# Optimization experiments

Hardware: AMD Instinct MI355X
Metric: run time of the kernel (lower is better)

The kernel has to match this reference:

```python
import jax, jax.numpy as jnp
from jax import lax
import numpy as np

BN_INV = 1.0 / np.sqrt(1.0 + 1e-5)  # eval-mode BatchNorm with running mean 0, var 1


def gather_points(x, idx):
    # x: [B, N, C]; idx: [B, ...] int -> [B, ..., C]
    bi = jnp.arange(x.shape[0]).reshape((x.shape[0],) + (1,) * (idx.ndim - 1))
    return x[bi, idx]


def fps(xyz, npoint):
    # furthest point sampling starting at index 0. xyz: [B, N, 3] -> [B, npoint] int32
    B, N, _ = xyz.shape

    def step(carry, _):
        dist, last = carry
        lx = jnp.take_along_axis(xyz, last[:, None, None], axis=1)  # [B,1,3]
        d = jnp.sum((xyz - lx) ** 2, axis=-1)                       # [B,N]
        dist = jnp.minimum(dist, d)
        nxt = jnp.argmax(dist, axis=-1).astype(jnp.int32)
        return (dist, nxt), nxt

    first = jnp.zeros((B,), jnp.int32)
    dist0 = jnp.full((B, N), 1e10, xyz.dtype)
    _, rest = lax.scan(step, (dist0, first), None, length=npoint - 1)
    return jnp.concatenate([first[None], rest], axis=0).T  # [B, npoint]


def ball_query(radius, nsample, xyz, new_xyz):
    # first nsample points (in index order) within radius of each query; pad with first hit
    N = xyz.shape[1]
    d2 = jnp.sum((new_xyz[:, :, None, :] - xyz[:, None, :, :]) ** 2, axis=-1)  # [B,S,N]
    mask = d2 < radius * radius
    key = jnp.where(mask, jnp.arange(N, dtype=jnp.int32), N)
    idx_sorted = jnp.sort(key, axis=-1)[..., :nsample]                          # [B,S,ns]
    cnt = jnp.sum(mask, axis=-1, keepdims=True)                                 # [B,S,1]
    idx = jnp.where(jnp.arange(nsample) < cnt, idx_sorted, idx_sorted[..., :1])
    return jnp.minimum(idx, N - 1)


def bn_relu(x, gamma, beta):
    # eval-mode BN (running mean 0 / var 1) + ReLU; channels on the last axis
    return jax.nn.relu(x * (gamma * BN_INV) + beta)


def sa_module(xyz, feats, npoint, radius, nsample, layers):
    # xyz [B,N,3], feats [B,C,N] -> (new_xyz [B,S,3], new_feats [B,Cout,S])
    fidx = fps(xyz, npoint)
    new_xyz = gather_points(xyz, fidx)                      # [B,S,3]
    gidx = ball_query(radius, nsample, xyz, new_xyz)        # [B,S,ns]
    g_xyz = gather_points(xyz, gidx) - new_xyz[:, :, None, :]   # [B,S,ns,3]
    g_feat = gather_points(jnp.swapaxes(feats, 1, 2), gidx)     # [B,S,ns,C]
    h = jnp.concatenate([g_xyz, g_feat], axis=-1)               # use_xyz=True
    for (w, g, b) in layers:                                    # shared MLP (1x1 conv2d+BN+ReLU)
        h = bn_relu(jnp.einsum('bsnc,oc->bsno', h, w), g, b)
    return new_xyz, jnp.swapaxes(jnp.max(h, axis=2), 1, 2)      # max-pool over nsample


def fp_module(unk_xyz, kn_xyz, unk_feats, kn_feats, layers):
    # three-NN weighted interpolation (squared distances, as the CUDA op) + unit conv MLP
    d2 = jnp.sum((unk_xyz[:, :, None, :] - kn_xyz[:, None, :, :]) ** 2, axis=-1)
    neg, idx = lax.top_k(-d2, 3)                 # 3 nearest known points
    w = 1.0 / (-neg + 1e-8)
    w = w / jnp.sum(w, axis=-1, keepdims=True)   # [B,Nu,3]
    kf = gather_points(jnp.swapaxes(kn_feats, 1, 2), idx)       # [B,Nu,3,C]
    interp = jnp.sum(kf * w[..., None], axis=2)                 # [B,Nu,C]
    h = jnp.concatenate([interp, jnp.swapaxes(unk_feats, 1, 2)], axis=-1)
    for (wt, g, b) in layers:
        h = bn_relu(jnp.einsum('bnc,oc->bno', h, wt), g, b)
    return jnp.swapaxes(h, 1, 2)                                # [B,Cout,Nu]


def setup_inputs() -> dict:
    key = jax.random.key(0)
    it = iter(jax.random.split(key, 80))
    B, N = 16, 4096
    d = {
        'xyz': jax.random.uniform(next(it), (B, N, 3), jnp.float32) * 0.3,
        'feats': jax.random.normal(next(it), (B, N, 3), jnp.float32),
    }
    specs = {'sa1': [(6, 64), (64, 128)], 'sa2': [(131, 128), (128, 256)],
             'sa3': [(259, 256), (256, 512)], 'fp3': [(768, 256), (256, 256)],
             'fp2': [(384, 128), (128, 128)], 'fp1': [(131, 128), (128, 128)]}
    for name, layers in specs.items():
        for i, (ci, co) in enumerate(layers):
            d[f'{name}_w{i}'] = jax.random.normal(next(it), (co, ci), jnp.float32) / np.sqrt(ci)
            d[f'{name}_g{i}'] = 1.0 + 0.1 * jax.random.normal(next(it), (co,), jnp.float32)
            d[f'{name}_b{i}'] = 0.1 * jax.random.normal(next(it), (co,), jnp.float32)
    d['fin_w'] = jax.random.normal(next(it), (512, 128), jnp.float32) / np.sqrt(128.0)
    d['fin_b'] = 0.1 * jax.random.normal(next(it), (512,), jnp.float32)
    d['fin_g'] = 1.0 + 0.1 * jax.random.normal(next(it), (512,), jnp.float32)
    d['fin_be'] = 0.1 * jax.random.normal(next(it), (512,), jnp.float32)
    return d


def reference(xyz, feats,
              sa1_w0, sa1_g0, sa1_b0, sa1_w1, sa1_g1, sa1_b1,
              sa2_w0, sa2_g0, sa2_b0, sa2_w1, sa2_g1, sa2_b1,
              sa3_w0, sa3_g0, sa3_b0, sa3_w1, sa3_g1, sa3_b1,
              fp3_w0, fp3_g0, fp3_b0, fp3_w1, fp3_g1, fp3_b1,
              fp2_w0, fp2_g0, fp2_b0, fp2_w1, fp2_g1, fp2_b1,
              fp1_w0, fp1_g0, fp1_b0, fp1_w1, fp1_g1, fp1_b1,
              fin_w, fin_b, fin_g, fin_be):
    f0 = jnp.swapaxes(feats, 1, 2)  # [B,3,N], channel-first like the torch module
    l1x, l1f = sa_module(xyz, f0, 256, 0.04, 16,
                         [(sa1_w0, sa1_g0, sa1_b0), (sa1_w1, sa1_g1, sa1_b1)])
    l2x, l2f = sa_module(l1x, l1f, 64, 0.08, 16,
                         [(sa2_w0, sa2_g0, sa2_b0), (sa2_w1, sa2_g1, sa2_b1)])
    l3x, l3f = sa_module(l2x, l2f, 16, 0.16, 16,
                         [(sa3_w0, sa3_g0, sa3_b0), (sa3_w1, sa3_g1, sa3_b1)])
    l2f = fp_module(l2x, l3x, l2f, l3f, [(fp3_w0, fp3_g0, fp3_b0), (fp3_w1, fp3_g1, fp3_b1)])
    l1f = fp_module(l1x, l2x, l1f, l2f, [(fp2_w0, fp2_g0, fp2_b0), (fp2_w1, fp2_g1, fp2_b1)])
    l0f = fp_module(xyz, l1x, f0, l1f, [(fp1_w0, fp1_g0, fp1_b0), (fp1_w1, fp1_g1, fp1_b1)])
    # final Conv1d(128->512, bias) + BN + ReLU
    h = jnp.einsum('bcn,oc->bon', l0f, fin_w) + fin_b[None, :, None]
    h = jax.nn.relu(h * (fin_g * BN_INV)[None, :, None] + fin_be[None, :, None])
    B, C, N = h.shape
    return jnp.swapaxes(h, 1, 2).reshape(B * N, C)  # un-batched per-point features
```

## Files before the change

### kernel.cpp

```cpp
#include <hip/hip_runtime.h>

#define DEVI __device__ __forceinline__
typedef unsigned long long u64;

static constexpr float BN_INV_F = 0.9999950000374997f;

DEVI float d2rn(float ax, float ay, float az, float bx, float by, float bz) {
    float dx = __fsub_rn(ax, bx), dy = __fsub_rn(ay, by), dz = __fsub_rn(az, bz);
    return __fadd_rn(__fadd_rn(__fmul_rn(dx, dx), __fmul_rn(dy, dy)), __fmul_rn(dz, dz));
}

DEVI u64 shfl_xor_u64(u64 x, int m) {
    unsigned lo = (unsigned)x, hi = (unsigned)(x >> 32);
    lo = (unsigned)__shfl_xor((int)lo, m, 64);
    hi = (unsigned)__shfl_xor((int)hi, m, 64);
    return ((u64)hi << 32) | lo;
}
DEVI u64 umin64(u64 a, u64 b) { return a < b ? a : b; }
DEVI u64 umax64(u64 a, u64 b) { return a > b ? a : b; }

template <int N, int NPOINT, int BS>
__global__ __launch_bounds__(BS) void fps_kernel(const float* __restrict__ xyz,
                                                 int* __restrict__ fidx) {
    constexpr int PPT = N / BS;
    constexpr int NW = BS / 64;
    __shared__ float xsx[N], xsy[N], xsz[N];
    __shared__ u64 wmax[2][NW > 0 ? NW : 1];
    const int t = threadIdx.x, b = blockIdx.x, lane = t & 63, wv = t >> 6;
    const float* xb = xyz + (size_t)b * N * 3;
    for (int p = t; p < N; p += BS) {
        xsx[p] = xb[p * 3]; xsy[p] = xb[p * 3 + 1]; xsz[p] = xb[p * 3 + 2];
    }
    float dist[PPT];
#pragma unroll
    for (int i = 0; i < PPT; ++i) dist[i] = 1e10f;
    if (t == 0) fidx[b * NPOINT] = 0;
    __syncthreads();
    float qx = xsx[0], qy = xsy[0], qz = xsz[0];
    for (int it = 1; it < NPOINT; ++it) {
        u64 best = 0ull;
#pragma unroll
        for (int i = 0; i < PPT; ++i) {
            int p = i * BS + t;
            float d = d2rn(xsx[p], xsy[p], xsz[p], qx, qy, qz);
            float nd = fminf(dist[i], d);
            dist[i] = nd;
            u64 pk = ((u64)__float_as_uint(nd) << 32) | (unsigned)(0xFFFFFFFFu - (unsigned)p);
            if (pk > best) best = pk;
        }
#pragma unroll
        for (int m = 1; m < 64; m <<= 1) best = umax64(best, shfl_xor_u64(best, m));
        if constexpr (NW > 1) {
            if (lane == 0) wmax[it & 1][wv] = best;
            __syncthreads();
            u64 m2 = wmax[it & 1][lane & (NW - 1)];
#pragma unroll
            for (int m = 1; m < NW; m <<= 1) m2 = umax64(m2, shfl_xor_u64(m2, m));
            best = m2;
        }
        int p = (int)(0xFFFFFFFFu - (unsigned)best);
        qx = xsx[p]; qy = xsy[p]; qz = xsz[p];
        if (t == 0) fidx[b * NPOINT + it] = p;
    }
}

template <int TR, int XSTR, int CI, int CO, int MODE>
DEVI void gemm_phase(float* __restrict__ Xs, float* __restrict__ Ws,
                     const float* __restrict__ W,
                     const float* __restrict__ sA, const float* __restrict__ sB,
                     const float* __restrict__ fbias,
                     float* __restrict__ gout, int r0,
                     unsigned* __restrict__ mp, int t) {
    constexpr int RT = TR / 16;
    constexpr int NCOL = (CO / 16 < 8) ? (CO / 16) : 8;
    constexpr int ROWS = 16 * NCOL;
    constexpr int CC = CO / ROWS;
    constexpr int CI16 = ((CI + 15) / 16) * 16;
    constexpr int NCH = CI16 / 8;
    constexpr int NQ = CC * NCH;
    constexpr int PRE = ROWS * 8 / 256;
    constexpr int XSTR4 = XSTR / 4;
    constexpr int AC = (MODE == 0) ? CC : 1;
    const int tx = t & 15, ty = t >> 4;
    float acc[AC][RT][NCOL];
    if constexpr (MODE == 0) {
#pragma unroll
        for (int a = 0; a < AC; ++a)
#pragma unroll
            for (int r = 0; r < RT; ++r)
#pragma unroll
                for (int i = 0; i < NCOL; ++i) acc[a][r][i] = 0.f;
    }
    float pre[PRE];
#pragma unroll
    for (int i = 0; i < PRE; ++i) {
        int e = t + 256 * i, row = e >> 3, kk = e & 7;
        pre[i] = (kk < CI) ? W[(size_t)row * CI + kk] : 0.f;
    }
#pragma unroll
    for (int i = 0; i < PRE; ++i) {
        int e = t + 256 * i;
        Ws[(e >> 3) * 12 + (e & 7)] = pre[i];
    }
#pragma unroll
    for (int cc = 0; cc < CC; ++cc) {
        if constexpr (MODE != 0) {
#pragma unroll
            for (int r = 0; r < RT; ++r)
#pragma unroll
                for (int i = 0; i < NCOL; ++i) acc[0][r][i] = 0.f;
        }
        for (int kc = 0; kc < NCH; ++kc) {
            const int qq = cc * NCH + kc, buf = kc & 1;
            __syncthreads();
            if (qq + 1 < NQ) {
                const int cn = (qq + 1) / NCH, kn = ((qq + 1) % NCH) * 8;
#pragma unroll
                for (int i = 0; i < PRE; ++i) {
                    int e = t + 256 * i, row = e >> 3, k = kn + (e & 7);
                    pre[i] = (k < CI) ? W[(size_t)(cn * ROWS + row) * CI + k] : 0.f;
                }
            }
            const float* wsb = Ws + buf * 1536;
#pragma unroll
            for (int k4i = 0; k4i < 2; ++k4i) {
                const int c4 = kc * 2 + k4i;
                float4 wv[NCOL];
#pragma unroll
                for (int i = 0; i < NCOL; ++i)
                    wv[i] = *(const float4*)&wsb[(tx + 16 * i) * 12 + k4i * 4];
#pragma unroll
                for (int r = 0; r < RT; ++r) {
                    float4 xv = *(const float4*)
                        &Xs[(((ty * RT + r) * XSTR4) + (c4 ^ (ty & 3))) * 4];
                    float* A;
                    if constexpr (MODE == 0) A = acc[cc][r]; else A = acc[0][r];
#pragma unroll
                    for (int i = 0; i < NCOL; ++i) {
                        A[i] = fmaf(xv.x, wv[i].x, A[i]);
                        A[i] = fmaf(xv.y, wv[i].y, A[i]);
                        A[i] = fmaf(xv.z, wv[i].z, A[i]);
                        A[i] = fmaf(xv.w, wv[i].w, A[i]);
                    }
                }
            }
            if (qq + 1 < NQ) {
                float* wsn = Ws + (buf ^ 1) * 1536;
#pragma unroll
                for (int i = 0; i < PRE; ++i) {
                    int e = t + 256 * i;
                    wsn[(e >> 3) * 12 + (e & 7)] = pre[i];
                }
            }
        }
        if constexpr (MODE == 1) {
#pragma unroll
            for (int i = 0; i < NCOL; ++i) {
                int c = cc * ROWS + tx + 16 * i;
                float bia = fbias[c], sc = sA[c] * BN_INV_F, be = sB[c];
#pragma unroll
                for (int r = 0; r < RT; ++r) {
                    float val = fmaxf(fmaf(acc[0][r][i] + bia, sc, be), 0.f);
                    gout[(size_t)(r0 + ty * RT + r) * CO + c] = val;
                }
            }
        } else if constexpr (MODE == 2) {
#pragma unroll
            for (int i = 0; i < NCOL; ++i) {
                int c = cc * ROWS + tx + 16 * i;
                float sc = sA[c] * BN_INV_F, bb = sB[c];
#pragma unroll
                for (int r = 0; r < RT; ++r) {
                    float val = fmaxf(fmaf(acc[0][r][i], sc, bb), 0.f);
                    atomicMax(&mp[((ty * RT + r) >> 4) * CO + c], __float_as_uint(val));
                }
            }
        }
    }
    if constexpr (MODE == 0) {
        __syncthreads();
#pragma unroll
        for (int cc = 0; cc < CC; ++cc)
#pragma unroll
            for (int i = 0; i < NCOL; ++i) {
                int c = cc * ROWS + tx + 16 * i;
                float sc = sA[c] * BN_INV_F, bb = sB[c];
#pragma unroll
                for (int r = 0; r < RT; ++r) {
                    int row = ty * RT + r;
                    Xs[(row * XSTR4 + ((c >> 2) ^ (ty & 3))) * 4 + (c & 3)] =
                        fmaxf(fmaf(acc[cc][r][i], sc, bb), 0.f);
                }
            }
        __syncthreads();
    }
}

template <int N, int S, int CIN, int C1, int C2, int TR>
__global__ __launch_bounds__(256) void sa_kernel(
    const float* __restrict__ xyz, const float* __restrict__ feats,
    const int* __restrict__ fidx,
    const float* __restrict__ w0, const float* __restrict__ g0, const float* __restrict__ b0,
    const float* __restrict__ w1, const float* __restrict__ g1, const float* __restrict__ b1,
    float* __restrict__ oxyz, float* __restrict__ ofeat, float r2) {
    constexpr int QPB = TR / 16;
    constexpr int C = 3 + CIN;
    constexpr int CI16 = ((C + 15) / 16) * 16;
    constexpr int XSTR = (CI16 > C1) ? CI16 : C1;
    constexpr int XSTR4 = XSTR / 4;
    constexpr int RTl = TR / 16;
    __shared__ __align__(16) float Xs[TR * XSTR];
    __shared__ __align__(16) float Ws[2 * 128 * 12];
    __shared__ int ids[QPB][16];
    __shared__ float qp[QPB][3];
    __shared__ unsigned mp[(TR / 16) * C2];
    const int t = threadIdx.x, lane = t & 63, wv = t >> 6;
    const int q0 = blockIdx.x * QPB;
    for (int q = wv; q < QPB; q += 4) {
        const int sq = q0 + q, bb = sq / S;
        const float* xb = xyz + (size_t)bb * N * 3;
        const int qi = fidx[sq];
        const float qx = xb[qi * 3], qy = xb[qi * 3 + 1], qz = xb[qi * 3 + 2];
        if (lane == 0) {
            qp[q][0] = qx; qp[q][1] = qy; qp[q][2] = qz;
            float* op = oxyz + (size_t)sq * 3;
            op[0] = qx; op[1] = qy; op[2] = qz;
        }
        int base = 0;
        for (int seg = 0; seg < N; seg += 64) {
            const int p = seg + lane;
            float d = d2rn(xb[p * 3], xb[p * 3 + 1], xb[p * 3 + 2], qx, qy, qz);
            bool hit = d < r2;
            u64 mask = __ballot(hit);
            int before = (int)__popcll(mask & ((1ull << lane) - 1ull));
            if (hit && base + before < 16) ids[q][base + before] = p;
            base += (int)__popcll(mask);
            if (base >= 16) break;
        }
        if (lane == 0) {
            int cnt = base < 16 ? base : 16;
            int first = ids[q][0];
            for (int r = cnt; r < 16; ++r) ids[q][r] = first;
        }
    }
    __syncthreads();
    if constexpr (CIN == 3) {
        for (int e = t; e < TR * CI16; e += 256) {
            int j = e / CI16, c = e % CI16;
            int q = j >> 4, p = ids[q][j & 15];
            int bb = (q0 + q) / S;
            float v = 0.f;
            if (c < 3) v = __fsub_rn(xyz[((size_t)bb * N + p) * 3 + c], qp[q][c]);
            else if (c < C) v = feats[((size_t)bb * N + p) * CIN + (c - 3)];
            Xs[(j * XSTR4 + ((c >> 2) ^ ((j / RTl) & 3))) * 4 + (c & 3)] = v;
        }
    } else {
        for (int e = t; e < TR * 16; e += 256) {
            int j = e / 16, ci = e % 16;
            int q = j >> 4, p = ids[q][j & 15];
            int bb = (q0 + q) / S;
            int c = (ci < 3) ? ci : (C + ci - 3);
            if (c >= CI16) continue;
            float v = (ci < 3) ? __fsub_rn(xyz[((size_t)bb * N + p) * 3 + ci], qp[q][ci]) : 0.f;
            Xs[(j * XSTR4 + ((c >> 2) ^ ((j / RTl) & 3))) * 4 + (c & 3)] = v;
        }
        for (int e = t; e < TR * (CIN / 4); e += 256) {
            int j = e / (CIN / 4), c4i = e % (CIN / 4);
            int q = j >> 4, p = ids[q][j & 15];
            int bb = (q0 + q) / S;
            float4 v = *(const float4*)&feats[((size_t)bb * N + p) * CIN + c4i * 4];
            int sw = (j / RTl) & 3;
            float vv[4] = {v.x, v.y, v.z, v.w};
#pragma unroll
            for (int u = 0; u < 4; ++u) {
                int c = 3 + c4i * 4 + u;
                Xs[(j * XSTR4 + ((c >> 2) ^ sw)) * 4 + (c & 3)] = vv[u];
            }
        }
    }
    gemm_phase<TR, XSTR, C, C1, 0>(Xs, Ws, w0, g0, b0, nullptr, nullptr, 0, nullptr, t);
    for (int e = t; e < (TR / 16) * C2; e += 256) mp[e] = 0u;
    gemm_phase<TR, XSTR, C1, C2, 2>(Xs, Ws, w1, g1, b1, nullptr, nullptr, 0, mp, t);
    __syncthreads();
    for (int e = t; e < QPB * C2; e += 256) {
        int q = e / C2, c = e % C2;
        ofeat[(size_t)(q0 + q) * C2 + c] = __uint_as_float(mp[e]);
    }
}

template <int M, int CK, int CU, int C1, int C2, int TR, bool FINAL>
__global__ __launch_bounds__(256) void fp_kernel(
    const float* __restrict__ uxyz, const float* __restrict__ kxyz,
    const float* __restrict__ ufeat, const float* __restrict__ kfeat,
    const float* __restrict__ w0, const float* __restrict__ g0, const float* __restrict__ b0,
    const float* __restrict__ w1, const float* __restrict__ g1, const float* __restrict__ b1,
    const float* __restrict__ fw, const float* __restrict__ fb,
    const float* __restrict__ fg, const float* __restrict__ fbe,
    float* __restrict__ out, int NU) {
    constexpr int CH = CK + CU;
    constexpr int CI16A = ((CH + 15) / 16) * 16;
    constexpr int XSTR = CI16A;
    constexpr int XSTR4 = XSTR / 4;
    constexpr int RT = TR / 16;
    __shared__ __align__(16) float Xs[TR * XSTR];
    __shared__ __align__(16) float Ws[2 * 128 * 12];
    __shared__ float kxs[M * 3];
    const int t = threadIdx.x, lane = t & 63, wv = t >> 6;
    const int r0 = blockIdx.x * TR;
    const int b = r0 / NU;
    for (int e = t; e < M * 3; e += 256) kxs[e] = kxyz[(size_t)b * M * 3 + e];
    __syncthreads();
    for (int j = wv; j < TR; j += 4) {
        const int r = r0 + j;
        const int sw = (j / RT) & 3;
        const float* up = uxyz + (size_t)r * 3;
        float ux = up[0], uy = up[1], uz = up[2];
        u64 a0 = ~0ull, a1 = ~0ull, a2 = ~0ull;
        for (int k = lane; k < M; k += 64) {
            float d = d2rn(kxs[k * 3], kxs[k * 3 + 1], kxs[k * 3 + 2], ux, uy, uz);
            u64 key = ((u64)__float_as_uint(d) << 32) | (unsigned)k;
            if (key < a0)      { a2 = a1; a1 = a0; a0 = key; }
            else if (key < a1) { a2 = a1; a1 = key; }
            else if (key < a2) { a2 = key; }
        }
#pragma unroll
        for (int m = 1; m < 64; m <<= 1) {
            u64 b0k = shfl_xor_u64(a0, m), b1k = shfl_xor_u64(a1, m), b2k = shfl_xor_u64(a2, m);
            u64 c0 = umin64(a0, b0k);
            u64 c1 = umin64(umax64(a0, b0k), umin64(a1, b1k));
            u64 c2 = umin64(umin64(umax64(a1, b0k), umax64(a0, b1k)), umin64(a2, b2k));
            a0 = c0; a1 = c1; a2 = c2;
        }
        int s0 = (int)(unsigned)a0, s1 = (int)(unsigned)a1, s2 = (int)(unsigned)a2;
        float d0 = __uint_as_float((unsigned)(a0 >> 32));
        float d1 = __uint_as_float((unsigned)(a1 >> 32));
        float dd2 = __uint_as_float((unsigned)(a2 >> 32));
        float wa = 1.0f / (d0 + 1e-8f), wb = 1.0f / (d1 + 1e-8f), wc = 1.0f / (dd2 + 1e-8f);
        float sum = (wa + wb) + wc;
        wa /= sum; wb /= sum; wc /= sum;
        const float* kb = kfeat + (size_t)b * M * CK;
        for (int c4 = lane; c4 < CK / 4; c4 += 64) {
            float4 va = *(const float4*)(kb + (size_t)s0 * CK + c4 * 4);
            float4 vb = *(const float4*)(kb + (size_t)s1 * CK + c4 * 4);
            float4 vc = *(const float4*)(kb + (size_t)s2 * CK + c4 * 4);
            float4 rr;
            rr.x = va.x * wa + vb.x * wb + vc.x * wc;
            rr.y = va.y * wa + vb.y * wb + vc.y * wc;
            rr.z = va.z * wa + vb.z * wb + vc.z * wc;
            rr.w = va.w * wa + vb.w * wb + vc.w * wc;
            *(float4*)&Xs[(j * XSTR4 + (c4 ^ sw)) * 4] = rr;
        }
        for (int c = CK + lane; c < CH; c += 64)
            Xs[(j * XSTR4 + ((c >> 2) ^ sw)) * 4 + (c & 3)] =
                ufeat[(size_t)r * CU + (c - CK)];
        for (int c = CH + lane; c < CI16A; c += 64)
            Xs[(j * XSTR4 + ((c >> 2) ^ sw)) * 4 + (c & 3)] = 0.f;
    }
    gemm_phase<TR, XSTR, CH, C1, 0>(Xs, Ws, w0, g0, b0, nullptr, nullptr, 0, nullptr, t);
    gemm_phase<TR, XSTR, C1, C2, 0>(Xs, Ws, w1, g1, b1, nullptr, nullptr, 0, nullptr, t);
    if constexpr (FINAL) {
        gemm_phase<TR, XSTR, C2, 512, 1>(Xs, Ws, fw, fg, fbe, fb, out, r0, nullptr, t);
    } else {
        for (int e = t; e < TR * C2; e += 256) {
            int j = e / C2, c = e % C2;
            int sw = (j / RT) & 3;
            out[(size_t)(r0 + j) * C2 + c] = Xs[(j * XSTR4 + ((c >> 2) ^ sw)) * 4 + (c & 3)];
        }
    }
}

extern "C" void kernel_launch(void* const* d_in, const int* in_sizes, int n_in,
                              void* d_out, int out_size, void* d_ws, size_t ws_size,
                              hipStream_t stream) {
    (void)in_sizes; (void)n_in; (void)out_size; (void)ws_size;
    const float* xyz   = (const float*)d_in[0];
    const float* feats = (const float*)d_in[1];
    const float* sa1_w0 = (const float*)d_in[2];
    const float* sa1_g0 = (const float*)d_in[3];
    const float* sa1_b0 = (const float*)d_in[4];
    const float* sa1_w1 = (const float*)d_in[5];
    const float* sa1_g1 = (const float*)d_in[6];
    const float* sa1_b1 = (const float*)d_in[7];
    const float* sa2_w0 = (const float*)d_in[8];
    const float* sa2_g0 = (const float*)d_in[9];
    const float* sa2_b0 = (const float*)d_in[10];
    const float* sa2_w1 = (const float*)d_in[11];
    const float* sa2_g1 = (const float*)d_in[12];
    const float* sa2_b1 = (const float*)d_in[13];
    const float* sa3_w0 = (const float*)d_in[14];
    const float* sa3_g0 = (const float*)d_in[15];
    const float* sa3_b0 = (const float*)d_in[16];
    const float* sa3_w1 = (const float*)d_in[17];
    const float* sa3_g1 = (const float*)d_in[18];
    const float* sa3_b1 = (const float*)d_in[19];
    const float* fp3_w0 = (const float*)d_in[20];
    const float* fp3_g0 = (const float*)d_in[21];
    const float* fp3_b0 = (const float*)d_in[22];
    const float* fp3_w1 = (const float*)d_in[23];
    const float* fp3_g1 = (const float*)d_in[24];
    const float* fp3_b1 = (const float*)d_in[25];
    const float* fp2_w0 = (const float*)d_in[26];
    const float* fp2_g0 = (const float*)d_in[27];
    const float* fp2_b0 = (const float*)d_in[28];
    const float* fp2_w1 = (const float*)d_in[29];
    const float* fp2_g1 = (const float*)d_in[30];
    const float* fp2_b1 = (const float*)d_in[31];
    const float* fp1_w0 = (const float*)d_in[32];
    const float* fp1_g0 = (const float*)d_in[33];
    const float* fp1_b0 = (const float*)d_in[34];
    const float* fp1_w1 = (const float*)d_in[35];
    const float* fp1_g1 = (const float*)d_in[36];
    const float* fp1_b1 = (const float*)d_in[37];
    const float* fin_w  = (const float*)d_in[38];
    const float* fin_b  = (const float*)d_in[39];
    const float* fin_g  = (const float*)d_in[40];
    const float* fin_be = (const float*)d_in[41];

    float* ws = (float*)d_ws;
    float* l1x  = ws;
    float* l1f  = l1x + 12288;
    float* l2x  = l1f + 524288;
    float* l2f  = l2x + 3072;
    float* l3x  = l2f + 262144;
    float* l3f  = l3x + 768;
    float* l2fb = l3f + 131072;
    float* l1fb = l2fb + 262144;
    int* fidx1 = (int*)(l1fb + 524288);
    int* fidx2 = fidx1 + 4096;
    int* fidx3 = fidx2 + 1024;

    const float R2_1 = (float)(0.04 * 0.04);
    const float R2_2 = (float)(0.08 * 0.08);
    const float R2_3 = (float)(0.16 * 0.16);

    fps_kernel<4096, 256, 512><<<16, 512, 0, stream>>>(xyz, fidx1);
    sa_kernel<4096, 256, 3, 64, 128, 64><<<16 * 256 / 4, 256, 0, stream>>>(
        xyz, feats, fidx1, sa1_w0, sa1_g0, sa1_b0, sa1_w1, sa1_g1, sa1_b1,
        l1x, l1f, R2_1);

    fps_kernel<256, 64, 256><<<16, 256, 0, stream>>>(l1x, fidx2);
    sa_kernel<256, 64, 128, 128, 256, 32><<<16 * 64 / 2, 256, 0, stream>>>(
        l1x, l1f, fidx2, sa2_w0, sa2_g0, sa2_b0, sa2_w1, sa2_g1, sa2_b1,
        l2x, l2f, R2_2);

    fps_kernel<64, 16, 64><<<16, 64, 0, stream>>>(l2x, fidx3);
    sa_kernel<64, 16, 256, 256, 512, 16><<<16 * 16, 256, 0, stream>>>(
        l2x, l2f, fidx3, sa3_w0, sa3_g0, sa3_b0, sa3_w1, sa3_g1, sa3_b1,
        l3x, l3f, R2_3);

    fp_kernel<16, 512, 256, 256, 256, 16, false><<<1024 / 16, 256, 0, stream>>>(
        l2x, l3x, l2f, l3f, fp3_w0, fp3_g0, fp3_b0, fp3_w1, fp3_g1, fp3_b1,
        nullptr, nullptr, nullptr, nullptr, l2fb, 64);

    fp_kernel<64, 256, 128, 128, 128, 16, false><<<4096 / 16, 256, 0, stream>>>(
        l1x, l2x, l1f, l2fb, fp2_w0, fp2_g0, fp2_b0, fp2_w1, fp2_g1, fp2_b1,
        nullptr, nullptr, nullptr, nullptr, l1fb, 256);

    fp_kernel<256, 128, 3, 128, 128, 64, true><<<65536 / 64, 256, 0, stream>>>(
        xyz, l1x, feats, l1fb, fp1_w0, fp1_g0, fp1_b0, fp1_w1, fp1_g1, fp1_b1,
        fin_w, fin_b, fin_g, fin_be, (float*)d_out, 4096);
}
```

Baseline: 903.2 us.

## Restructure SA/FP kernels: side-channel xyz, larger tiles, split final conv kernel

Splits the generic templated kernels into per-stage kernels and handles the 3 relative-xyz channels as a separate rank-3 side update, so the main GEMM K stays a multiple of 16 without padding. Larger row tiles are used for sa2 and for fp1, which now has its own kernel with a 4-lane cooperative 3-NN search. The final 128->512 conv moves into a separate in-place kernel over the output buffer. The inner GEMM loop is changed to preload all X vectors before the FMAs. Gains come from better weight reuse and less padding work, at the cost of an extra launch and a write-then-reread of the 512-wide output.

```diff
diff --git a/kernel.cpp b/kernel.cpp
--- a/kernel.cpp
+++ b/kernel.cpp
@@ -20,8 +20,7 @@
 DEVI u64 umax64(u64 a, u64 b) { return a > b ? a : b; }
 
 template <int N, int NPOINT, int BS>
-__global__ __launch_bounds__(BS) void fps_kernel(const float* __restrict__ xyz,
-                                                 int* __restrict__ fidx) {
+DEVI void fps_impl(const float* __restrict__ xyz, int* __restrict__ fidx) {
     constexpr int PPT = N / BS;
     constexpr int NW = BS / 64;
     __shared__ float xsx[N], xsy[N], xsz[N];
@@ -64,24 +63,29 @@
     }
 }
 
-template <int TR, int XSTR, int CI, int CO, int MODE>
+__global__ __launch_bounds__(512) void fps1_kernel(const float* __restrict__ x, int* __restrict__ f) { fps_impl<4096, 256, 512>(x, f); }
+__global__ __launch_bounds__(256) void fps2_kernel(const float* __restrict__ x, int* __restrict__ f) { fps_impl<256, 64, 256>(x, f); }
+__global__ __launch_bounds__(64)  void fps3_kernel(const float* __restrict__ x, int* __restrict__ f) { fps_impl<64, 16, 64>(x, f); }
+
+template <int TR, int XSTR, int KMAIN, int CIM, int CIF, int MOFF, int CO, int MODE,
+          bool SIDE, int SOFF, int OSTR>
 DEVI void gemm_phase(float* __restrict__ Xs, float* __restrict__ Ws,
                      const float* __restrict__ W,
                      const float* __restrict__ sA, const float* __restrict__ sB,
                      const float* __restrict__ fbias,
                      float* __restrict__ gout, int r0,
-                     unsigned* __restrict__ mp, int t) {
+                     unsigned* __restrict__ mp, const float* __restrict__ side, int t) {
     constexpr int RT = TR / 16;
     constexpr int NCOL = (CO / 16 < 8) ? (CO / 16) : 8;
     constexpr int ROWS = 16 * NCOL;
     constexpr int CC = CO / ROWS;
-    constexpr int CI16 = ((CI + 15) / 16) * 16;
-    constexpr int NCH = CI16 / 8;
+    constexpr int NCH = KMAIN / 8;
     constexpr int NQ = CC * NCH;
-    constexpr int PRE = ROWS * 8 / 256;
+    constexpr int PRE = ROWS / 32;
     constexpr int XSTR4 = XSTR / 4;
     constexpr int AC = (MODE == 0) ? CC : 1;
     const int tx = t & 15, ty = t >> 4;
+    const int swz = ty & 3;
     float acc[AC][RT][NCOL];
     if constexpr (MODE == 0) {
 #pragma unroll
@@ -95,7 +99,7 @@
 #pragma unroll
     for (int i = 0; i < PRE; ++i) {
         int e = t + 256 * i, row = e >> 3, kk = e & 7;
-        pre[i] = (kk < CI) ? W[(size_t)row * CI + kk] : 0.f;
+        pre[i] = (kk < CIM) ? W[(size_t)row * CIF + MOFF + kk] : 0.f;
     }
 #pragma unroll
     for (int i = 0; i < PRE; ++i) {
@@ -118,10 +122,10 @@
 #pragma unroll
                 for (int i = 0; i < PRE; ++i) {
                     int e = t + 256 * i, row = e >> 3, k = kn + (e & 7);
-                    pre[i] = (k < CI) ? W[(size_t)(cn * ROWS + row) * CI + k] : 0.f;
-                }
-            }
-            const float* wsb = Ws + buf * 1536;
+                    pre[i] = (k < CIM) ? W[(size_t)(cn * ROWS + row) * CIF + MOFF + k] : 0.f;
+                }
+            }
+            const float* wsb = Ws + buf * (ROWS * 12);
 #pragma unroll
             for (int k4i = 0; k4i < 2; ++k4i) {
                 const int c4 = kc * 2 + k4i;
@@ -129,23 +133,23 @@
 #pragma unroll
                 for (int i = 0; i < NCOL; ++i)
                     wv[i] = *(const float4*)&wsb[(tx + 16 * i) * 12 + k4i * 4];
-#pragma unroll
-                for (int r = 0; r < RT; ++r) {
-                    float4 xv = *(const float4*)
-                        &Xs[(((ty * RT + r) * XSTR4) + (c4 ^ (ty & 3))) * 4];
-                    float* A;
-                    if constexpr (MODE == 0) A = acc[cc][r]; else A = acc[0][r];
+                float4 xv[RT];
+#pragma unroll
+                for (int r = 0; r < RT; ++r)
+                    xv[r] = *(const float4*)&Xs[((ty * RT + r) * XSTR4 + (c4 ^ swz)) * 4];
+#pragma unroll
+                for (int r = 0; r < RT; ++r)
 #pragma unroll
                     for (int i = 0; i < NCOL; ++i) {
-                        A[i] = fmaf(xv.x, wv[i].x, A[i]);
-                        A[i] = fmaf(xv.y, wv[i].y, A[i]);
-                        A[i] = fmaf(xv.z, wv[i].z, A[i]);
-                        A[i] = fmaf(xv.w, wv[i].w, A[i]);
+                        const int a = (MODE == 0) ? cc : 0;
+                        acc[a][r][i] = fmaf(xv[r].x, wv[i].x, acc[a][r][i]);
+                        acc[a][r][i] = fmaf(xv[r].y, wv[i].y, acc[a][r][i]);
+                        acc[a][r][i] = fmaf(xv[r].z, wv[i].z, acc[a][r][i]);
+                        acc[a][r][i] = fmaf(xv[r].w, wv[i].w, acc[a][r][i]);
                     }
-                }
             }
             if (qq + 1 < NQ) {
-                float* wsn = Ws + (buf ^ 1) * 1536;
+                float* wsn = Ws + (buf ^ 1) * (ROWS * 12);
 #pragma unroll
                 for (int i = 0; i < PRE; ++i) {
                     int e = t + 256 * i;
@@ -157,11 +161,12 @@
 #pragma unroll
             for (int i = 0; i < NCOL; ++i) {
                 int c = cc * ROWS + tx + 16 * i;
-                float bia = fbias[c], sc = sA[c] * BN_INV_F, be = sB[c];
+                float bia = fbias ? fbias[c] : 0.f;
+                float sc = sA[c] * BN_INV_F, be = sB[c];
 #pragma unroll
                 for (int r = 0; r < RT; ++r) {
                     float val = fmaxf(fmaf(acc[0][r][i] + bia, sc, be), 0.f);
-                    gout[(size_t)(r0 + ty * RT + r) * CO + c] = val;
+                    gout[(size_t)(r0 + ty * RT + r) * OSTR + c] = val;
                 }
             }
         } else if constexpr (MODE == 2) {
@@ -178,9 +183,25 @@
         }
     }
     if constexpr (MODE == 0) {
+        if constexpr (SIDE) {
+#pragma unroll
+            for (int cc = 0; cc < AC; ++cc)
+#pragma unroll
+                for (int i = 0; i < NCOL; ++i) {
+                    int c = cc * ROWS + tx + 16 * i;
+#pragma unroll
+                    for (int j = 0; j < 3; ++j) {
+                        float wj = W[(size_t)c * CIF + SOFF + j];
+#pragma unroll
+                        for (int r = 0; r < RT; ++r)
+                            acc[cc][r][i] = fmaf(side[(ty * RT + r) * 3 + j], wj,
+                                                 acc[cc][r][i]);
+                    }
+                }
+        }
         __syncthreads();
 #pragma unroll
-        for (int cc = 0; cc < CC; ++cc)
+        for (int cc = 0; cc < AC; ++cc)
 #pragma unroll
             for (int i = 0; i < NCOL; ++i) {
                 int c = cc * ROWS + tx + 16 * i;
@@ -188,7 +209,7 @@
 #pragma unroll
                 for (int r = 0; r < RT; ++r) {
                     int row = ty * RT + r;
-                    Xs[(row * XSTR4 + ((c >> 2) ^ (ty & 3))) * 4 + (c & 3)] =
+                    Xs[(row * XSTR4 + ((c >> 2) ^ swz)) * 4 + (c & 3)] =
                         fmaxf(fmaf(acc[cc][r][i], sc, bb), 0.f);
                 }
             }
@@ -196,24 +217,24 @@
     }
 }
 
-template <int N, int S, int CIN, int C1, int C2, int TR>
-__global__ __launch_bounds__(256) void sa_kernel(
-    const float* __restrict__ xyz, const float* __restrict__ feats,
-    const int* __restrict__ fidx,
-    const float* __restrict__ w0, const float* __restrict__ g0, const float* __restrict__ b0,
-    const float* __restrict__ w1, const float* __restrict__ g1, const float* __restrict__ b1,
-    float* __restrict__ oxyz, float* __restrict__ ofeat, float r2) {
+template <int N, int S, int CIN, int C1, int C2, int TR, bool USE_SIDE>
+DEVI void sa_impl(const float* __restrict__ xyz, const float* __restrict__ feats,
+                  const int* __restrict__ fidx,
+                  const float* __restrict__ w0, const float* __restrict__ g0, const float* __restrict__ b0,
+                  const float* __restrict__ w1, const float* __restrict__ g1, const float* __restrict__ b1,
+                  float* __restrict__ oxyz, float* __restrict__ ofeat, float r2) {
     constexpr int QPB = TR / 16;
-    constexpr int C = 3 + CIN;
-    constexpr int CI16 = ((C + 15) / 16) * 16;
-    constexpr int XSTR = (CI16 > C1) ? CI16 : C1;
+    constexpr int CIF = 3 + CIN;
+    constexpr int KMAIN = USE_SIDE ? CIN : 16;
+    constexpr int XSTR = (KMAIN > C1) ? KMAIN : C1;
     constexpr int XSTR4 = XSTR / 4;
-    constexpr int RTl = TR / 16;
+    constexpr int RT = TR / 16;
     __shared__ __align__(16) float Xs[TR * XSTR];
     __shared__ __align__(16) float Ws[2 * 128 * 12];
     __shared__ int ids[QPB][16];
     __shared__ float qp[QPB][3];
-    __shared__ unsigned mp[(TR / 16) * C2];
+    __shared__ unsigned mp[QPB * C2];
+    __shared__ float side[USE_SIDE ? TR * 3 : 4];
     const int t = threadIdx.x, lane = t & 63, wv = t >> 6;
     const int q0 = blockIdx.x * QPB;
     for (int q = wv; q < QPB; q += 4) {
@@ -244,62 +265,66 @@
         }
     }
     __syncthreads();
-    if constexpr (CIN == 3) {
-        for (int e = t; e < TR * CI16; e += 256) {
-            int j = e / CI16, c = e % CI16;
+    if constexpr (!USE_SIDE) {
+        for (int e = t; e < TR * 16; e += 256) {
+            int j = e >> 4, c = e & 15;
             int q = j >> 4, p = ids[q][j & 15];
             int bb = (q0 + q) / S;
             float v = 0.f;
             if (c < 3) v = __fsub_rn(xyz[((size_t)bb * N + p) * 3 + c], qp[q][c]);
-            else if (c < C) v = feats[((size_t)bb * N + p) * CIN + (c - 3)];
-            Xs[(j * XSTR4 + ((c >> 2) ^ ((j / RTl) & 3))) * 4 + (c & 3)] = v;
+            else if (c < 6) v = feats[((size_t)bb * N + p) * CIN + (c - 3)];
+            Xs[(j * XSTR4 + ((c >> 2) ^ ((j / RT) & 3))) * 4 + (c & 3)] = v;
         }
     } else {
-        for (int e = t; e < TR * 16; e += 256) {
-            int j = e / 16, ci = e % 16;
+        constexpr int C4N = CIN / 4;
+        for (int e = t; e < TR * C4N; e += 256) {
+            int j = e / C4N, c4 = e % C4N;
             int q = j >> 4, p = ids[q][j & 15];
             int bb = (q0 + q) / S;
-            int c = (ci < 3) ? ci : (C + ci - 3);
-            if (c >= CI16) continue;
-            float v = (ci < 3) ? __fsub_rn(xyz[((size_t)bb * N + p) * 3 + ci], qp[q][ci]) : 0.f;
-            Xs[(j * XSTR4 + ((c >> 2) ^ ((j / RTl) & 3))) * 4 + (c & 3)] = v;
-        }
-        for (int e = t; e < TR * (CIN / 4); e += 256) {
-            int j = e / (CIN / 4), c4i = e % (CIN / 4);
+            float4 v = *(const float4*)&feats[((size_t)bb * N + p) * CIN + c4 * 4];
+            *(float4*)&Xs[(j * XSTR4 + (c4 ^ ((j / RT) & 3))) * 4] = v;
+        }
+        for (int e = t; e < TR * 3; e += 256) {
+            int j = e / 3, c = e % 3;
             int q = j >> 4, p = ids[q][j & 15];
             int bb = (q0 + q) / S;
-            float4 v = *(const float4*)&feats[((size_t)bb * N + p) * CIN + c4i * 4];
-            int sw = (j / RTl) & 3;
-            float vv[4] = {v.x, v.y, v.z, v.w};
-#pragma unroll
-            for (int u = 0; u < 4; ++u) {
-                int c = 3 + c4i * 4 + u;
-                Xs[(j * XSTR4 + ((c >> 2) ^ sw)) * 4 + (c & 3)] = vv[u];
-            }
-        }
-    }
-    gemm_phase<TR, XSTR, C, C1, 0>(Xs, Ws, w0, g0, b0, nullptr, nullptr, 0, nullptr, t);
-    for (int e = t; e < (TR / 16) * C2; e += 256) mp[e] = 0u;
-    gemm_phase<TR, XSTR, C1, C2, 2>(Xs, Ws, w1, g1, b1, nullptr, nullptr, 0, mp, t);
+            side[e] = __fsub_rn(xyz[((size_t)bb * N + p) * 3 + c], qp[q][c]);
+        }
+    }
+    for (int e = t; e < QPB * C2; e += 256) mp[e] = 0u;
+    gemm_phase<TR, XSTR, KMAIN, (USE_SIDE ? CIN : 6), CIF, (USE_SIDE ? 3 : 0),
+               C1, 0, USE_SIDE, 0, 0>(Xs, Ws, w0, g0, b0, nullptr, nullptr, 0,
+                                      nullptr, side, t);
+    gemm_phase<TR, XSTR, C1, C1, C1, 0, C2, 2, false, 0, 0>(
+        Xs, Ws, w1, g1, b1, nullptr, nullptr, 0, mp, nullptr, t);
     __syncthreads();
-    for (int e = t; e < QPB * C2; e += 256) {
-        int q = e / C2, c = e % C2;
-        ofeat[(size_t)(q0 + q) * C2 + c] = __uint_as_float(mp[e]);
-    }
-}
-
-template <int M, int CK, int CU, int C1, int C2, int TR, bool FINAL>
-__global__ __launch_bounds__(256) void fp_kernel(
-    const float* __restrict__ uxyz, const float* __restrict__ kxyz,
-    const float* __restrict__ ufeat, const float* __restrict__ kfeat,
-    const float* __restrict__ w0, const float* __restrict__ g0, const float* __restrict__ b0,
-    const float* __restrict__ w1, const float* __restrict__ g1, const float* __restrict__ b1,
-    const float* __restrict__ fw, const float* __restrict__ fb,
-    const float* __restrict__ fg, const float* __restrict__ fbe,
-    float* __restrict__ out, int NU) {
+    for (int e = t; e < QPB * C2; e += 256)
+        ofeat[(size_t)q0 * C2 + e] = __uint_as_float(mp[e]);
+}
+
+#define SA_ARGS const float* __restrict__ xyz, const float* __restrict__ feats, \
+                const int* __restrict__ fidx, \
+                const float* __restrict__ w0, const float* __restrict__ g0, const float* __restrict__ b0, \
+                const float* __restrict__ w1, const float* __restrict__ g1, const float* __restrict__ b1, \
+                float* __restrict__ oxyz, float* __restrict__ ofeat, float r2
+__global__ __launch_bounds__(256) void sa1_kernel(SA_ARGS) {
+    sa_impl<4096, 256, 3, 64, 128, 64, false>(xyz, feats, fidx, w0, g0, b0, w1, g1, b1, oxyz, ofeat, r2);
+}
+__global__ __launch_bounds__(256) void sa2_kernel(SA_ARGS) {
+    sa_impl<256, 64, 128, 128, 256, 64, true>(xyz, feats, fidx, w0, g0, b0, w1, g1, b1, oxyz, ofeat, r2);
+}
+__global__ __launch_bounds__(256) void sa3_kernel(SA_ARGS) {
+    sa_impl<64, 16, 256, 256, 512, 16, true>(xyz, feats, fidx, w0, g0, b0, w1, g1, b1, oxyz, ofeat, r2);
+}
+
+template <int M, int CK, int CU, int C1, int C2, int TR>
+DEVI void fp_impl(const float* __restrict__ uxyz, const float* __restrict__ kxyz,
+                  const float* __restrict__ ufeat, const float* __restrict__ kfeat,
+                  const float* __restrict__ w0, const float* __restrict__ g0, const float* __restrict__ b0,
+                  const float* __restrict__ w1, const float* __restrict__ g1, const float* __restrict__ b1,
+                  float* __restrict__ out, int NU) {
     constexpr int CH = CK + CU;
-    constexpr int CI16A = ((CH + 15) / 16) * 16;
-    constexpr int XSTR = CI16A;
+    constexpr int XSTR = CH;
     constexpr int XSTR4 = XSTR / 4;
     constexpr int RT = TR / 16;
     __shared__ __align__(16) float Xs[TR * XSTR];
@@ -350,21 +375,184 @@
             rr.w = va.w * wa + vb.w * wb + vc.w * wc;
             *(float4*)&Xs[(j * XSTR4 + (c4 ^ sw)) * 4] = rr;
         }
-        for (int c = CK + lane; c < CH; c += 64)
-            Xs[(j * XSTR4 + ((c >> 2) ^ sw)) * 4 + (c & 3)] =
-                ufeat[(size_t)r * CU + (c - CK)];
-        for (int c = CH + lane; c < CI16A; c += 64)
-            Xs[(j * XSTR4 + ((c >> 2) ^ sw)) * 4 + (c & 3)] = 0.f;
-    }
-    gemm_phase<TR, XSTR, CH, C1, 0>(Xs, Ws, w0, g0, b0, nullptr, nullptr, 0, nullptr, t);
-    gemm_phase<TR, XSTR, C1, C2, 0>(Xs, Ws, w1, g1, b1, nullptr, nullptr, 0, nullptr, t);
-    if constexpr (FINAL) {
-        gemm_phase<TR, XSTR, C2, 512, 1>(Xs, Ws, fw, fg, fbe, fb, out, r0, nullptr, t);
-    } else {
-        for (int e = t; e < TR * C2; e += 256) {
-            int j = e / C2, c = e % C2;
-            int sw = (j / RT) & 3;
-            out[(size_t)(r0 + j) * C2 + c] = Xs[(j * XSTR4 + ((c >> 2) ^ sw)) * 4 + (c & 3)];
+        for (int c4 = CK / 4 + lane; c4 < CH / 4; c4 += 64) {
+            float4 v = *(const float4*)&ufeat[(size_t)r * CU + (c4 * 4 - CK)];
+            *(float4*)&Xs[(j * XSTR4 + (c4 ^ sw)) * 4] = v;
+        }
+    }
+    gemm_phase<TR, XSTR, CH, CH, CH, 0, C1, 0, false, 0, 0>(
+        Xs, Ws, w0, g0, b0, nullptr, nullptr, 0, nullptr, nullptr, t);
+    gemm_phase<TR, XSTR, C1, C1, C1, 0, C2, 1, false, 0, C2>(
+        Xs, Ws, w1, g1, b1, nullptr, out, r0, nullptr, nullptr, t);
+}
+
+#define FP_ARGS const float* __restrict__ uxyz, const float* __restrict__ kxyz, \
+                const float* __restrict__ ufeat, const float* __restrict__ kfeat, \
+                const float* __restrict__ w0, const float* __restrict__ g0, const float* __restrict__ b0, \
+                const float* __restrict__ w1, const float* __restrict__ g1, const float* __restrict__ b1, \
+                float* __restrict__ out, int NU
+__global__ __launch_bounds__(256) void fp3_kernel(FP_ARGS) {
+    fp_impl<16, 512, 256, 256, 256, 16>(uxyz, kxyz, ufeat, kfeat, w0, g0, b0, w1, g1, b1, out, NU);
+}
+__global__ __launch_bounds__(256) void fp2_kernel(FP_ARGS) {
+    fp_impl<64, 256, 128, 128, 128, 16>(uxyz, kxyz, ufeat, kfeat, w0, g0, b0, w1, g1, b1, out, NU);
+}
+
+__global__ __launch_bounds__(256) void fp1_mlp_kernel(
+    const float* __restrict__ uxyz, const float* __restrict__ kxyz,
+    const float* __restrict__ ufeat3, const float* __restrict__ kfeat,
+    const float* __restrict__ w0, const float* __restrict__ g0, const float* __restrict__ b0,
+    const float* __restrict__ w1, const float* __restrict__ g1, const float* __restrict__ b1,
+    float* __restrict__ out) {
+    constexpr int TR = 128, M = 256, CK = 128;
+    __shared__ __align__(16) float Xs[TR * 128];
+    __shared__ __align__(16) float Ws[2 * 128 * 12];
+    __shared__ float side[TR * 3];
+    __shared__ float wgt2[TR * 2];
+    __shared__ unsigned pidx[TR];
+    const int t = threadIdx.x;
+    const int r0 = blockIdx.x * TR;
+    const int b = r0 >> 12;
+    for (int e = t; e < TR * 3; e += 256) side[e] = ufeat3[(size_t)r0 * 3 + e];
+    const int g = t >> 2, sub = t & 3;
+    const float* kb3 = kxyz + (size_t)b * M * 3;
+    for (int row = g; row < TR; row += 64) {
+        const float* up = uxyz + (size_t)(r0 + row) * 3;
+        float ux = up[0], uy = up[1], uz = up[2];
+        u64 a0 = ~0ull, a1 = ~0ull, a2 = ~0ull;
+        for (int k = sub; k < M; k += 4) {
+            float d = d2rn(kb3[k * 3], kb3[k * 3 + 1], kb3[k * 3 + 2], ux, uy, uz);
+            u64 key = ((u64)__float_as_uint(d) << 32) | (unsigned)k;
+            if (key < a0)      { a2 = a1; a1 = a0; a0 = key; }
+            else if (key < a1) { a2 = a1; a1 = key; }
+            else if (key < a2) { a2 = key; }
+        }
+#pragma unroll
+        for (int m = 1; m < 4; m <<= 1) {
+            u64 b0k = shfl_xor_u64(a0, m), b1k = shfl_xor_u64(a1, m), b2k = shfl_xor_u64(a2, m);
+            u64 c0 = umin64(a0, b0k);
+            u64 c1 = umin64(umax64(a0, b0k), umin64(a1, b1k));
+            u64 c2 = umin64(umin64(umax64(a1, b0k), umax64(a0, b1k)), umin64(a2, b2k));
+            a0 = c0; a1 = c1; a2 = c2;
+        }
+        if (sub == 0) {
+            unsigned s0 = (unsigned)a0 & 255u, s1 = (unsigned)a1 & 255u, s2 = (unsigned)a2 & 255u;
+            float d0 = __uint_as_float((unsigned)(a0 >> 32));
+            float d1 = __uint_as_float((unsigned)(a1 >> 32));
+            float dd2 = __uint_as_float((unsigned)(a2 >> 32));
+            float wa = 1.0f / (d0 + 1e-8f), wb = 1.0f / (d1 + 1e-8f), wc = 1.0f / (dd2 + 1e-8f);
+            float sum = (wa + wb) + wc;
+            wa /= sum; wb /= sum;
+            pidx[row] = s0 | (s1 << 8) | (s2 << 16);
+            wgt2[row * 2] = wa; wgt2[row * 2 + 1] = wb;
+        }
+    }
+    __syncthreads();
+    const float* kfb = kfeat + (size_t)b * M * CK;
+    for (int e = t; e < TR * 32; e += 256) {
+        int j = e >> 5, c4 = e & 31;
+        unsigned u = pidx[j];
+        int s0 = u & 255, s1 = (u >> 8) & 255, s2 = (u >> 16) & 255;
+        float wa = wgt2[j * 2], wb = wgt2[j * 2 + 1], wc = 1.0f - wa - wb;
+        float4 va = *(const float4*)(kfb + (size_t)s0 * CK + c4 * 4);
+        float4 vb = *(const float4*)(kfb + (size_t)s1 * CK + c4 * 4);
+        float4 vc = *(const float4*)(kfb + (size_t)s2 * CK + c4 * 4);
+        float4 rr;
+        rr.x = va.x * wa + vb.x * wb + vc.x * wc;
+        rr.y = va.y * wa + vb.y * wb + vc.y * wc;
+        rr.z = va.z * wa + vb.z * wb + vc.z * wc;
+        rr.w = va.w * wa + vb.w * wb + vc.w * wc;
+        *(float4*)&Xs[(j * 32 + (c4 ^ ((j >> 3) & 3))) * 4] = rr;
+    }
+    gemm_phase<TR, 128, 128, 128, 131, 0, 128, 0, true, 128, 0>(
+        Xs, Ws, w0, g0, b0, nullptr, nullptr, 0, nullptr, side, t);
+    gemm_phase<TR, 128, 128, 128, 128, 0, 128, 1, false, 0, 512>(
+        Xs, Ws, w1, g1, b1, nullptr, out, r0, nullptr, nullptr, t);
+}
+
+__global__ __launch_bounds__(256) void fin_kernel(
+    float* io,
+    const float* __restrict__ fw, const float* __restrict__ fb,
+    const float* __restrict__ fg, const float* __restrict__ fbe) {
+    __shared__ __align__(16) float Xs[128 * 128];
+    __shared__ __align__(16) float Ws[2 * 128 * 12];
+    const int t = threadIdx.x, tx = t & 15, ty = t >> 4;
+    const int r0 = blockIdx.x * 128;
+    const int swz = ty & 3;
+    for (int e = t; e < 128 * 32; e += 256) {
+        int j = e >> 5, c4 = e & 31;
+        float4 v = *(const float4*)&io[(size_t)(r0 + j) * 512 + c4 * 4];
+        *(float4*)&Xs[(j * 32 + (c4 ^ ((j >> 3) & 3))) * 4] = v;
+    }
+    for (int nt = 0; nt < 4; ++nt) {
+        const int c0 = nt * 128;
+        float acc[8][8];
+#pragma unroll
+        for (int r = 0; r < 8; ++r)
+#pragma unroll
+            for (int i = 0; i < 8; ++i) acc[r][i] = 0.f;
+        float wpre[4];
+#pragma unroll
+        for (int i = 0; i < 4; ++i) {
+            int e = t + 256 * i, row = e >> 3, kk = e & 7;
+            wpre[i] = fw[(size_t)(c0 + row) * 128 + kk];
+        }
+#pragma unroll
+        for (int i = 0; i < 4; ++i) {
+            int e = t + 256 * i;
+            Ws[(e >> 3) * 12 + (e & 7)] = wpre[i];
+        }
+        for (int kc = 0; kc < 16; ++kc) {
+            const int buf = kc & 1;
+            __syncthreads();
+            if (kc < 15) {
+                const int kn = (kc + 1) * 8;
+#pragma unroll
+                for (int i = 0; i < 4; ++i) {
+                    int e = t + 256 * i, row = e >> 3, kk = e & 7;
+                    wpre[i] = fw[(size_t)(c0 + row) * 128 + kn + kk];
+                }
+            }
+            const float* wsb = Ws + buf * 1536;
+#pragma unroll
+            for (int k4i = 0; k4i < 2; ++k4i) {
+                const int c4 = kc * 2 + k4i;
+                float4 wv[8];
+#pragma unroll
+                for (int i = 0; i < 8; ++i)
+                    wv[i] = *(const float4*)&wsb[(tx + 16 * i) * 12 + k4i * 4];
+                float4 xv[8];
+#pragma unroll
+                for (int r = 0; r < 8; ++r)
+                    xv[r] = *(const float4*)&Xs[((ty * 8 + r) * 32 + (c4 ^ swz)) * 4];
+#pragma unroll
+                for (int r = 0; r < 8; ++r)
+#pragma unroll
+                    for (int i = 0; i < 8; ++i) {
+                        acc[r][i] = fmaf(xv[r].x, wv[i].x, acc[r][i]);
+                        acc[r][i] = fmaf(xv[r].y, wv[i].y, acc[r][i]);
+                        acc[r][i] = fmaf(xv[r].z, wv[i].z, acc[r][i]);
+                        acc[r][i] = fmaf(xv[r].w, wv[i].w, acc[r][i]);
+                    }
+            }
+            if (kc < 15) {
+                float* wsn = Ws + (buf ^ 1) * 1536;
+#pragma unroll
+                for (int i = 0; i < 4; ++i) {
+                    int e = t + 256 * i;
+                    wsn[(e >> 3) * 12 + (e & 7)] = wpre[i];
+                }
+            }
+        }
+#pragma unroll
+        for (int i = 0; i < 8; ++i) {
+            int c = c0 + tx + 16 * i;
+            float bia = fb[c], sc = fg[c] * BN_INV_F, be = fbe[c];
+#pragma unroll
+            for (int r = 0; r < 8; ++r) {
+                float val = fmaxf(fmaf(acc[r][i] + bia, sc, be), 0.f);
+                io[(size_t)(r0 + ty * 8 + r) * 512 + c] = val;
+            }
         }
     }
 }
@@ -433,30 +621,33 @@
     const float R2_2 = (float)(0.08 * 0.08);
     const float R2_3 = (float)(0.16 * 0.16);
 
-    fps_kernel<4096, 256, 512><<<16, 512, 0, stream>>>(xyz, fidx1);
-    sa_kernel<4096, 256, 3, 64, 128, 64><<<16 * 256 / 4, 256, 0, stream>>>(
+    fps1_kernel<<<16, 512, 0, stream>>>(xyz, fidx1);
+    sa1_kernel<<<1024, 256, 0, stream>>>(
         xyz, feats, fidx1, sa1_w0, sa1_g0, sa1_b0, sa1_w1, sa1_g1, sa1_b1,
         l1x, l1f, R2_1);
 
-    fps_kernel<256, 64, 256><<<16, 256, 0, stream>>>(l1x, fidx2);
-    sa_kernel<256, 64, 128, 128, 256, 32><<<16 * 64 / 2, 256, 0, stream>>>(
+    fps2_kernel<<<16, 256, 0, stream>>>(l1x, fidx2);
+    sa2_kernel<<<256, 256, 0, stream>>>(
         l1x, l1f, fidx2, sa2_w0, sa2_g0, sa2_b0, sa2_w1, sa2_g1, sa2_b1,
         l2x, l2f, R2_2);
 
-    fps_kernel<64, 16, 64><<<16, 64, 0, stream>>>(l2x, fidx3);
-    sa_kernel<64, 16, 256, 256, 512, 16><<<16 * 16, 256, 0, stream>>>(
+    fps3_kernel<<<16, 64, 0, stream>>>(l2x, fidx3);
+    sa3_kernel<<<256, 256, 0, stream>>>(
         l2x, l2f, fidx3, sa3_w0, sa3_g0, sa3_b0, sa3_w1, sa3_g1, sa3_b1,
         l3x, l3f, R2_3);
 
-    fp_kernel<16, 512, 256, 256, 256, 16, false><<<1024 / 16, 256, 0, stream>>>(
+    fp3_kernel<<<64, 256, 0, stream>>>(
         l2x, l3x, l2f, l3f, fp3_w0, fp3_g0, fp3_b0, fp3_w1, fp3_g1, fp3_b1,
-        nullptr, nullptr, nullptr, nullptr, l2fb, 64);
-
-    fp_kernel<64, 256, 128, 128, 128, 16, false><<<4096 / 16, 256, 0, stream>>>(
+        l2fb, 64);
+
+    fp2_kernel<<<256, 256, 0, stream>>>(
         l1x, l2x, l1f, l2fb, fp2_w0, fp2_g0, fp2_b0, fp2_w1, fp2_g1, fp2_b1,
-        nullptr, nullptr, nullptr, nullptr, l1fb, 256);
-
-    fp_kernel<256, 128, 3, 128, 128, 64, true><<<65536 / 64, 256, 0, stream>>>(
+        l1fb, 256);
+
+    fp1_mlp_kernel<<<512, 256, 0, stream>>>(
         xyz, l1x, feats, l1fb, fp1_w0, fp1_g0, fp1_b0, fp1_w1, fp1_g1, fp1_b1,
-        fin_w, fin_b, fin_g, fin_be, (float*)d_out, 4096);
-}
+        (float*)d_out);
+
+    fin_kernel<<<512, 256, 0, stream>>>(
+        (float*)d_out, fin_w, fin_b, fin_g, fin_be);
+}
```

Result: faster. 842.9 us (-6.7%).
